# Performance work log

Hardware: AMD Instinct MI355X
Metric: run time of the kernel (lower is better)

## Reference

```python
import jax, jax.numpy as jnp
import numpy as np

LEVELS = 256
# round(d*cos(a)), round(d*sin(a)) for d=1, angles 0, pi/4, pi/2, 3pi/4 (torch defaults)
SHIFTS = [(1, 0), (1, 1), (0, 1), (-1, 1)]


def _glcm(gray):
    # gray: (n, h, w) int32 in [0, LEVELS-1]
    n = gray.shape[0]
    B = LEVELS * LEVELS
    cooc = []
    for dx, dy in SHIFTS:  # fixed small set of angles
        shifted = jnp.roll(gray, shift=(dx, dy), axis=(1, 2))
        joint = (gray * LEVELS + shifted).reshape(n, -1)  # (n, h*w)
        vmin = joint.min()
        vmax = joint.max()
        # faithful torch.histc binning: B equal-width bins over [vmin, vmax],
        # values == vmax fall in last bin (handled by clip)
        scale = B / jnp.maximum((vmax - vmin).astype(jnp.float32), 1.0)
        bins = jnp.clip(
            jnp.floor((joint - vmin).astype(jnp.float32) * scale).astype(jnp.int32),
            0, B - 1)
        bidx = jnp.broadcast_to(jnp.arange(n)[:, None], joint.shape)
        hist = jnp.zeros((n, B), jnp.float32).at[bidx, bins].add(1.0)
        cooc.append(hist.reshape(n, LEVELS, LEVELS).sum(axis=0))
    co = jnp.stack(cooc, axis=-1)            # (L, L, A)
    co = co + jnp.swapaxes(co, 0, 1)          # symmetric=True
    glcm = co / co.sum()                      # normalize over ALL dims incl. angles (as torch)
    return glcm[:, :, None, :]                # (L, L, n_dist=1, A)


def _contrast(glcm):
    i = jnp.arange(LEVELS, dtype=jnp.float32)
    w = (i[:, None] - i[None, :]) ** 2        # (L, L) contrast weights
    return jnp.sum(glcm * w[:, :, None, None], axis=(0, 1))  # (n_dist, A)


def _loss(original, generated):
    og = jax.lax.stop_gradient(
        jnp.round(original.mean(axis=1) * (LEVELS - 1)).astype(jnp.int32))
    gg = jax.lax.stop_gradient(
        jnp.round(generated.mean(axis=1) * (LEVELS - 1)).astype(jnp.int32))
    return jnp.mean(jnp.abs(_contrast(_glcm(og)) - _contrast(_glcm(gg))))


def setup_inputs() -> dict:
    key = jax.random.key(0)
    k1, k2 = jax.random.split(key)
    shape = (16, 3, 512, 512)
    return {
        "original": jax.random.uniform(k1, shape, dtype=jnp.float32),
        "generated": jax.random.uniform(k2, shape, dtype=jnp.float32),
    }


def reference(original, generated):
    return _loss(original, generated)
```

## Files before the change

### kernel.cpp

```cpp
#include <hip/hip_runtime.h>

#define W 512
#define NPIX 4194304

union Bytes { uint4 v; unsigned char b[16]; };

__device__ __forceinline__ unsigned char gray1(float a, float b, float c) {
    return (unsigned char)__float2int_rn(((a + b + c) / 3.0f) * 255.0f);
}

__global__ __launch_bounds__(256, 8) void k1_gray_minmax(
    const float4* __restrict__ og, const float4* __restrict__ gg,
    uchar4* __restrict__ gray, unsigned int* __restrict__ blockmm) {
    int inp = blockIdx.y;
    int img = blockIdx.x >> 6;
    int r0 = (blockIdx.x & 63) << 3;
    const float4* src = (inp ? gg : og) + (size_t)img * 3 * 65536;
    uchar4* gout = gray + (size_t)inp * (NPIX / 4) + img * 65536;

    __shared__ unsigned char lds[10 * W];
    uchar4* lds4 = (uchar4*)lds;
#pragma unroll
    for (int j = 0; j < 5; ++j) {
        int q = threadIdx.x + j * 256;
        int i = q >> 7, quad = q & 127;
        int ir = (r0 - 1 + i) & 511;
        float4 a = src[(size_t)ir * 128 + quad];
        float4 b = src[65536 + (size_t)ir * 128 + quad];
        float4 c = src[131072 + (size_t)ir * 128 + quad];
        uchar4 r;
        r.x = gray1(a.x, b.x, c.x);
        r.y = gray1(a.y, b.y, c.y);
        r.z = gray1(a.z, b.z, c.z);
        r.w = gray1(a.w, b.w, c.w);
        lds4[q] = r;
        if (i >= 1 && i <= 8) gout[ir * 128 + quad] = r;
    }
    __syncthreads();

    int lr = 1 + (threadIdx.x >> 5);
    int c0 = (threadIdx.x & 31) << 4;
    const unsigned char* Lm = lds + (lr - 1) * W;
    const unsigned char* Lc = lds + lr * W;
    const unsigned char* Lp = lds + (lr + 1) * W;
    Bytes rm, rc, rp;
    rm.v = *(const uint4*)(Lm + c0);
    rc.v = *(const uint4*)(Lc + c0);
    rp.v = *(const uint4*)(Lp + c0);
    int cp = (c0 - 1) & 511;
    unsigned char pm = Lm[cp], pc = Lc[cp], pp = Lp[cp];

    unsigned int lmin[4] = {~0u, ~0u, ~0u, ~0u};
    unsigned int lmax[4] = {0u, 0u, 0u, 0u};
#pragma unroll
    for (int j = 0; j < 16; ++j) {
        unsigned int base = ((unsigned int)rc.b[j]) << 8;
        unsigned int v0 = base + rm.b[j];
        unsigned int v1 = base + (j ? rm.b[j - 1] : pm);
        unsigned int v2 = base + (j ? rc.b[j - 1] : pc);
        unsigned int v3 = base + (j ? rp.b[j - 1] : pp);
        lmin[0] = min(lmin[0], v0); lmax[0] = max(lmax[0], v0);
        lmin[1] = min(lmin[1], v1); lmax[1] = max(lmax[1], v1);
        lmin[2] = min(lmin[2], v2); lmax[2] = max(lmax[2], v2);
        lmin[3] = min(lmin[3], v3); lmax[3] = max(lmax[3], v3);
    }
#pragma unroll
    for (int off = 32; off > 0; off >>= 1) {
#pragma unroll
        for (int s = 0; s < 4; ++s) {
            lmin[s] = min(lmin[s], (unsigned int)__shfl_down((int)lmin[s], off));
            lmax[s] = max(lmax[s], (unsigned int)__shfl_down((int)lmax[s], off));
        }
    }
    __shared__ unsigned int wmin[4][4], wmax[4][4];
    int wave = threadIdx.x >> 6;
    if ((threadIdx.x & 63) == 0) {
#pragma unroll
        for (int s = 0; s < 4; ++s) { wmin[wave][s] = lmin[s]; wmax[wave][s] = lmax[s]; }
    }
    __syncthreads();
    if (threadIdx.x < 4) {
        int s = threadIdx.x;
        unsigned int mn = min(min(wmin[0][s], wmin[1][s]), min(wmin[2][s], wmin[3][s]));
        unsigned int mx = max(max(wmax[0][s], wmax[1][s]), max(wmax[2][s], wmax[3][s]));
        blockmm[inp * 8192 + s * 1024 + blockIdx.x] = mn;
        blockmm[inp * 8192 + (4 + s) * 1024 + blockIdx.x] = mx;
    }
}

__global__ __launch_bounds__(256, 8) void k2_contrast(
    const uchar4* __restrict__ gray, const unsigned int* __restrict__ blockmm,
    unsigned int* __restrict__ partial) {
    int inp = blockIdx.y;
    int img = blockIdx.x >> 6;
    int r0 = (blockIdx.x & 63) << 3;

    __shared__ unsigned char lds[10 * W];
    __shared__ unsigned int mmfin[8];
    uchar4* lds4 = (uchar4*)lds;
    const uchar4* gin = gray + (size_t)inp * (NPIX / 4) + img * 65536;

#pragma unroll
    for (int j = 0; j < 5; ++j) {
        int q = threadIdx.x + j * 256;
        int i = q >> 7, quad = q & 127;
        int ir = (r0 - 1 + i) & 511;
        lds4[q] = gin[ir * 128 + quad];
    }
    {
        int s8 = threadIdx.x >> 5, lane = threadIdx.x & 31;
        const unsigned int* mb = blockmm + inp * 8192 + s8 * 1024;
        unsigned int v = mb[lane];
#pragma unroll
        for (int k = 1; k < 32; ++k) {
            unsigned int u = mb[lane + k * 32];
            v = (s8 < 4) ? min(v, u) : max(v, u);
        }
#pragma unroll
        for (int off = 16; off > 0; off >>= 1) {
            unsigned int u = (unsigned int)__shfl_down((int)v, off, 32);
            v = (s8 < 4) ? min(v, u) : max(v, u);
        }
        if (lane == 0) mmfin[s8] = v;
    }
    __syncthreads();

    unsigned int vm[4]; float scale[4];
#pragma unroll
    for (int s = 0; s < 4; ++s) {
        vm[s] = mmfin[s];
        scale[s] = 65536.0f / fmaxf((float)(mmfin[4 + s] - vm[s]), 1.0f);
    }

    int lr = 1 + (threadIdx.x >> 5);
    int c0 = (threadIdx.x & 31) << 4;
    const unsigned char* Lm = lds + (lr - 1) * W;
    const unsigned char* Lc = lds + lr * W;
    const unsigned char* Lp = lds + (lr + 1) * W;
    Bytes rm, rc, rp;
    rm.v = *(const uint4*)(Lm + c0);
    rc.v = *(const uint4*)(Lc + c0);
    rp.v = *(const uint4*)(Lp + c0);
    int cp = (c0 - 1) & 511;
    unsigned char pm = Lm[cp], pc = Lc[cp], pp = Lp[cp];

    unsigned int acc[4] = {0u, 0u, 0u, 0u};
#pragma unroll
    for (int j = 0; j < 16; ++j) {
        unsigned int base = ((unsigned int)rc.b[j]) << 8;
        unsigned int v[4];
        v[0] = base + rm.b[j];
        v[1] = base + (j ? rm.b[j - 1] : pm);
        v[2] = base + (j ? rc.b[j - 1] : pc);
        v[3] = base + (j ? rp.b[j - 1] : pp);
#pragma unroll
        for (int s = 0; s < 4; ++s) {
            int b = (int)((float)(v[s] - vm[s]) * scale[s]);
            b = b > 65535 ? 65535 : b;
            int d = (b >> 8) - (b & 255);
            acc[s] += (unsigned int)(d * d);
        }
    }
#pragma unroll
    for (int off = 32; off > 0; off >>= 1)
#pragma unroll
        for (int s = 0; s < 4; ++s)
            acc[s] += (unsigned int)__shfl_down((int)acc[s], off);

    __shared__ unsigned int wsum[4][4];
    int wave = threadIdx.x >> 6;
    if ((threadIdx.x & 63) == 0) {
#pragma unroll
        for (int s = 0; s < 4; ++s) wsum[wave][s] = acc[s];
    }
    __syncthreads();
    if (threadIdx.x < 4) {
        int s = threadIdx.x;
        unsigned int tot = wsum[0][s] + wsum[1][s] + wsum[2][s] + wsum[3][s];
        partial[(inp * 4 + s) * 1024 + blockIdx.x] = tot;
    }
}

__global__ __launch_bounds__(256) void k3_loss(
    const unsigned int* __restrict__ partial, float* __restrict__ out) {
    int c = threadIdx.x >> 5;
    int lane = threadIdx.x & 31;
    const unsigned int* p = partial + c * 1024;
    double acc = 0.0;
#pragma unroll
    for (int k = 0; k < 32; ++k) acc += (double)p[lane + k * 32];
#pragma unroll
    for (int off = 16; off > 0; off >>= 1) acc += __shfl_down(acc, off, 32);
    __shared__ double cs[8];
    if (lane == 0) cs[c] = acc;
    __syncthreads();
    if (threadIdx.x == 0) {
        double r = 0.0;
        for (int a = 0; a < 4; ++a) {
            double co = 2.0 * cs[a]     / 33554432.0;
            double cg = 2.0 * cs[4 + a] / 33554432.0;
            r += fabs(co - cg);
        }
        out[0] = (float)(r * 0.25);
    }
}

extern "C" void kernel_launch(void* const* d_in, const int* in_sizes, int n_in,
                              void* d_out, int out_size, void* d_ws, size_t ws_size,
                              hipStream_t stream) {
    const float4* og = (const float4*)d_in[0];
    const float4* gg = (const float4*)d_in[1];
    float* out = (float*)d_out;

    unsigned int* blockmm = (unsigned int*)d_ws;
    unsigned int* partial = blockmm + 16384;
    uchar4* gray = (uchar4*)((char*)d_ws + 131072);

    dim3 grid(1024, 2);
    k1_gray_minmax<<<grid, 256, 0, stream>>>(og, gg, gray, blockmm);
    k2_contrast<<<grid, 256, 0, stream>>>(gray, blockmm, partial);
    k3_loss<<<1, 256, 0, stream>>>(partial, out);
}
```

Before: 45.09 us.

## Split gray conversion from min/max and drop LDS halo staging

Result: faster. 43.57 us (-3.4%).

```diff
diff --git a/kernel.cpp b/kernel.cpp
--- a/kernel.cpp
+++ b/kernel.cpp
@@ -4,51 +4,58 @@
 #define NPIX 4194304
 
 union Bytes { uint4 v; unsigned char b[16]; };
+union B8 { uint2 v; unsigned char b[8]; };
 
 __device__ __forceinline__ unsigned char gray1(float a, float b, float c) {
     return (unsigned char)__float2int_rn(((a + b + c) / 3.0f) * 255.0f);
 }
 
-__global__ __launch_bounds__(256, 8) void k1_gray_minmax(
+__global__ __launch_bounds__(256, 8) void k1_gray(
     const float4* __restrict__ og, const float4* __restrict__ gg,
-    uchar4* __restrict__ gray, unsigned int* __restrict__ blockmm) {
+    uint2* __restrict__ gray2) {
     int inp = blockIdx.y;
-    int img = blockIdx.x >> 6;
-    int r0 = (blockIdx.x & 63) << 3;
-    const float4* src = (inp ? gg : og) + (size_t)img * 3 * 65536;
-    uchar4* gout = gray + (size_t)inp * (NPIX / 4) + img * 65536;
-
-    __shared__ unsigned char lds[10 * W];
-    uchar4* lds4 = (uchar4*)lds;
-#pragma unroll
-    for (int j = 0; j < 5; ++j) {
-        int q = threadIdx.x + j * 256;
-        int i = q >> 7, quad = q & 127;
-        int ir = (r0 - 1 + i) & 511;
-        float4 a = src[(size_t)ir * 128 + quad];
-        float4 b = src[65536 + (size_t)ir * 128 + quad];
-        float4 c = src[131072 + (size_t)ir * 128 + quad];
-        uchar4 r;
-        r.x = gray1(a.x, b.x, c.x);
-        r.y = gray1(a.y, b.y, c.y);
-        r.z = gray1(a.z, b.z, c.z);
-        r.w = gray1(a.w, b.w, c.w);
-        lds4[q] = r;
-        if (i >= 1 && i <= 8) gout[ir * 128 + quad] = r;
-    }
-    __syncthreads();
-
-    int lr = 1 + (threadIdx.x >> 5);
-    int c0 = (threadIdx.x & 31) << 4;
-    const unsigned char* Lm = lds + (lr - 1) * W;
-    const unsigned char* Lc = lds + lr * W;
-    const unsigned char* Lp = lds + (lr + 1) * W;
+    int t = blockIdx.x * 256 + threadIdx.x;
+    const float4* src = inp ? gg : og;
+    int img = t >> 15;
+    int u = t & 32767;
+    size_t b = (size_t)img * 196608 + ((size_t)u << 1);
+
+    float4 a0 = src[b],          a1 = src[b + 1];
+    float4 b0 = src[b + 65536],  b1 = src[b + 65537];
+    float4 c0 = src[b + 131072], c1 = src[b + 131073];
+
+    B8 r;
+    r.b[0] = gray1(a0.x, b0.x, c0.x);
+    r.b[1] = gray1(a0.y, b0.y, c0.y);
+    r.b[2] = gray1(a0.z, b0.z, c0.z);
+    r.b[3] = gray1(a0.w, b0.w, c0.w);
+    r.b[4] = gray1(a1.x, b1.x, c1.x);
+    r.b[5] = gray1(a1.y, b1.y, c1.y);
+    r.b[6] = gray1(a1.z, b1.z, c1.z);
+    r.b[7] = gray1(a1.w, b1.w, c1.w);
+    gray2[(size_t)inp * 524288 + t] = r.v;
+}
+
+__global__ __launch_bounds__(256, 8) void k2_minmax(
+    const unsigned char* __restrict__ gray,
+    unsigned int* __restrict__ blockmm) {
+    int inp = blockIdx.y;
+    const unsigned char* g = gray + (size_t)inp * NPIX;
+    int t = blockIdx.x * 256 + threadIdx.x;
+    int img = t >> 14;
+    int p = t & 16383;
+    int r = p >> 5;
+    int c0 = (p & 31) << 4;
+    const unsigned char* gn = g + (img << 18);
+    int rm1 = (r - 1) & 511, rp1 = (r + 1) & 511, cp = (c0 - 1) & 511;
+
     Bytes rm, rc, rp;
-    rm.v = *(const uint4*)(Lm + c0);
-    rc.v = *(const uint4*)(Lc + c0);
-    rp.v = *(const uint4*)(Lp + c0);
-    int cp = (c0 - 1) & 511;
-    unsigned char pm = Lm[cp], pc = Lc[cp], pp = Lp[cp];
+    rm.v = *(const uint4*)(gn + (rm1 << 9) + c0);
+    rc.v = *(const uint4*)(gn + (r   << 9) + c0);
+    rp.v = *(const uint4*)(gn + (rp1 << 9) + c0);
+    unsigned char pm = gn[(rm1 << 9) | cp];
+    unsigned char pc = gn[(r   << 9) | cp];
+    unsigned char pp = gn[(rp1 << 9) | cp];
 
     unsigned int lmin[4] = {~0u, ~0u, ~0u, ~0u};
     unsigned int lmax[4] = {0u, 0u, 0u, 0u};
@@ -88,25 +95,29 @@
     }
 }
 
-__global__ __launch_bounds__(256, 8) void k2_contrast(
-    const uchar4* __restrict__ gray, const unsigned int* __restrict__ blockmm,
+__global__ __launch_bounds__(256, 8) void k3_contrast(
+    const unsigned char* __restrict__ gray,
+    const unsigned int* __restrict__ blockmm,
     unsigned int* __restrict__ partial) {
     int inp = blockIdx.y;
-    int img = blockIdx.x >> 6;
-    int r0 = (blockIdx.x & 63) << 3;
-
-    __shared__ unsigned char lds[10 * W];
+    const unsigned char* g = gray + (size_t)inp * NPIX;
+    int t = blockIdx.x * 256 + threadIdx.x;
+    int img = t >> 14;
+    int p = t & 16383;
+    int r = p >> 5;
+    int c0 = (p & 31) << 4;
+    const unsigned char* gn = g + (img << 18);
+    int rm1 = (r - 1) & 511, rp1 = (r + 1) & 511, cp = (c0 - 1) & 511;
+
+    Bytes rm, rc, rp;
+    rm.v = *(const uint4*)(gn + (rm1 << 9) + c0);
+    rc.v = *(const uint4*)(gn + (r   << 9) + c0);
+    rp.v = *(const uint4*)(gn + (rp1 << 9) + c0);
+    unsigned char pm = gn[(rm1 << 9) | cp];
+    unsigned char pc = gn[(r   << 9) | cp];
+    unsigned char pp = gn[(rp1 << 9) | cp];
+
     __shared__ unsigned int mmfin[8];
-    uchar4* lds4 = (uchar4*)lds;
-    const uchar4* gin = gray + (size_t)inp * (NPIX / 4) + img * 65536;
-
-#pragma unroll
-    for (int j = 0; j < 5; ++j) {
-        int q = threadIdx.x + j * 256;
-        int i = q >> 7, quad = q & 127;
-        int ir = (r0 - 1 + i) & 511;
-        lds4[q] = gin[ir * 128 + quad];
-    }
     {
         int s8 = threadIdx.x >> 5, lane = threadIdx.x & 31;
         const unsigned int* mb = blockmm + inp * 8192 + s8 * 1024;
@@ -131,18 +142,6 @@
         vm[s] = mmfin[s];
         scale[s] = 65536.0f / fmaxf((float)(mmfin[4 + s] - vm[s]), 1.0f);
     }
-
-    int lr = 1 + (threadIdx.x >> 5);
-    int c0 = (threadIdx.x & 31) << 4;
-    const unsigned char* Lm = lds + (lr - 1) * W;
-    const unsigned char* Lc = lds + lr * W;
-    const unsigned char* Lp = lds + (lr + 1) * W;
-    Bytes rm, rc, rp;
-    rm.v = *(const uint4*)(Lm + c0);
-    rc.v = *(const uint4*)(Lc + c0);
-    rp.v = *(const uint4*)(Lp + c0);
-    int cp = (c0 - 1) & 511;
-    unsigned char pm = Lm[cp], pc = Lc[cp], pp = Lp[cp];
 
     unsigned int acc[4] = {0u, 0u, 0u, 0u};
 #pragma unroll
@@ -181,7 +180,7 @@
     }
 }
 
-__global__ __launch_bounds__(256) void k3_loss(
+__global__ __launch_bounds__(256) void k4_loss(
     const unsigned int* __restrict__ partial, float* __restrict__ out) {
     int c = threadIdx.x >> 5;
     int lane = threadIdx.x & 31;
@@ -214,10 +213,12 @@
 
     unsigned int* blockmm = (unsigned int*)d_ws;
     unsigned int* partial = blockmm + 16384;
-    uchar4* gray = (uchar4*)((char*)d_ws + 131072);
-
-    dim3 grid(1024, 2);
-    k1_gray_minmax<<<grid, 256, 0, stream>>>(og, gg, gray, blockmm);
-    k2_contrast<<<grid, 256, 0, stream>>>(gray, blockmm, partial);
-    k3_loss<<<1, 256, 0, stream>>>(partial, out);
-}
+    unsigned char* gray = (unsigned char*)d_ws + 131072;
+
+    dim3 g1(2048, 2);
+    k1_gray<<<g1, 256, 0, stream>>>(og, gg, (uint2*)gray);
+    dim3 g2(1024, 2);
+    k2_minmax<<<g2, 256, 0, stream>>>(gray, blockmm);
+    k3_contrast<<<g2, 256, 0, stream>>>(gray, blockmm, partial);
+    k4_loss<<<1, 256, 0, stream>>>(partial, out);
+}
```
